# Kernel optimization log

Measured on AMD Instinct MI355X. Metric: run time of the kernel, lower is better.

Reference implementation:

```python
import jax, jax.numpy as jnp
import numpy as np


def setup_inputs() -> dict:
    key = jax.random.key(0)
    k1, k2, k3, k4 = jax.random.split(key, 4)
    B, T, E, D = 4, 4096, 2048, 128
    x = jax.random.normal(k1, (B, T, E), dtype=jnp.float32)
    # nn.Linear(E, D, bias=False): y = x @ W where W is [E, D]
    scale = 1.0 / np.sqrt(E)
    Wq = jax.random.normal(k2, (E, D), dtype=jnp.float32) * scale
    Wk = jax.random.normal(k3, (E, D), dtype=jnp.float32) * scale
    Wv = jax.random.normal(k4, (E, D), dtype=jnp.float32) * scale
    return {"x": x, "Wq": Wq, "Wk": Wk, "Wv": Wv}


def reference(x, Wq, Wk, Wv):
    # Single attention head, prefill path (kv_cache=None, T_q == T_k).
    D = Wq.shape[1]
    Q = jnp.einsum('bte,ed->btd', x, Wq)
    K = jnp.einsum('bte,ed->btd', x, Wk)
    V = jnp.einsum('bte,ed->btd', x, Wv)
    scores = jnp.einsum('bqd,bkd->bqk', Q, K) / jnp.sqrt(jnp.float32(D))
    T = x.shape[1]
    causal = jnp.tril(jnp.ones((T, T), dtype=bool))  # [T_q, T_k]
    scores = jnp.where(causal[None, :, :], scores, -jnp.inf)
    attn = jax.nn.softmax(scores, axis=-1)
    out = jnp.einsum('bqk,bkd->bqd', attn, V)
    return out
```

## Files before the change

### kernel.cpp

```cpp
#include <hip/hip_runtime.h>
#include <hip/hip_bf16.h>

typedef short bf16x8 __attribute__((ext_vector_type(8)));
typedef float f32x4  __attribute__((ext_vector_type(4)));

#define T_SEQ 4096
#define NB    4
#define E_DIM 2048
#define D_DIM 128
#define M_TOT (NB * T_SEQ)
#define NCHUNK 4
#define CHUNK_KT 16
#define SM_SHIFT 12.0f

__device__ __forceinline__ ushort f2bf(float f) {
  union { float f; unsigned u; } c; c.f = f;
  unsigned u = c.u;
  unsigned r = (u + 0x7FFFu + ((u >> 16) & 1u)) >> 16;
  return (ushort)r;
}
__device__ __forceinline__ float bf2f(ushort u) {
  union { unsigned u; float f; } c; c.u = ((unsigned)u) << 16;
  return c.f;
}
__device__ __forceinline__ bf16x8 cvt8(const float4& lo, const float4& hi) {
  union { __hip_bfloat162 h; ushort u[2]; } t;
  union { ushort u[8]; bf16x8 v; } r;
  t.h = __float22bfloat162_rn(make_float2(lo.x, lo.y)); r.u[0] = t.u[0]; r.u[1] = t.u[1];
  t.h = __float22bfloat162_rn(make_float2(lo.z, lo.w)); r.u[2] = t.u[0]; r.u[3] = t.u[1];
  t.h = __float22bfloat162_rn(make_float2(hi.x, hi.y)); r.u[4] = t.u[0]; r.u[5] = t.u[1];
  t.h = __float22bfloat162_rn(make_float2(hi.z, hi.w)); r.u[6] = t.u[0]; r.u[7] = t.u[1];
  return r.v;
}

__device__ __forceinline__ void gl2lds16(const void* g, void* l) {
  __builtin_amdgcn_global_load_lds(
      (const __attribute__((address_space(1))) unsigned int*)g,
      (__attribute__((address_space(3))) unsigned int*)l, 16, 0, 0);
}

__global__ __launch_bounds__(256) void build_wt(const float* __restrict__ Wq,
                                                const float* __restrict__ Wk,
                                                const float* __restrict__ Wv,
                                                ushort* __restrict__ Wt) {
  __shared__ ushort tile[64][72];
  const int tid = threadIdx.x;
  const int k0 = blockIdx.x * 64, n0 = blockIdx.y * 64, o = blockIdx.z;
  const float* W = (o == 0) ? Wq : ((o == 1) ? Wk : Wv);
  for (int i = 0; i < 4; i++) {
    int c = tid + i * 256;
    int r = c >> 4, c4 = (c & 15) * 4;
    float4 v = *(const float4*)(W + (size_t)(k0 + r) * D_DIM + n0 + c4);
    ushort4 b4;
    b4.x = f2bf(v.x); b4.y = f2bf(v.y); b4.z = f2bf(v.z); b4.w = f2bf(v.w);
    *(ushort4*)(&tile[r][c4]) = b4;
  }
  __syncthreads();
  for (int i = 0; i < 2; i++) {
    int c = tid + i * 256;
    int nn = c >> 3, k8 = (c & 7) * 8;
    ushort tmp[8];
    for (int j = 0; j < 8; j++) tmp[j] = tile[k8 + j][nn];
    *(uint4*)(Wt + (size_t)((o << 7) + n0 + nn) * E_DIM + k0 + k8) = *(const uint4*)tmp;
  }
}

__global__ __launch_bounds__(256, 4) void qkv_gemm(const float* __restrict__ x,
                                                   const ushort* __restrict__ Wt,
                                                   ushort* __restrict__ Q,
                                                   ushort* __restrict__ K,
                                                   ushort* __restrict__ Vt) {
  __shared__ ushort As[2][64 * 64];
  __shared__ ushort Bs[2][96 * 64];

  const int tid  = threadIdx.x;
  const int wave = tid >> 6, lane = tid & 63;
  const int quad = lane >> 4, l16 = lane & 15;
  const int wm = wave >> 1, wn = wave & 1;
  const int m0 = blockIdx.x * 64;
  const int n0 = blockIdx.y * 96;

  f32x4 acc[2][3] = {};

  const int s_ = wave * 64 + lane;
  const int n_ = s_ >> 3, p_ = s_ & 7;

  const int ar_ = tid >> 2, aq4_ = tid & 3;
  const float* xrow = x + (size_t)(m0 + ar_) * E_DIM + aq4_ * 16;

#define DMA_B(k0_, buf_)                                                        \
  _Pragma("unroll")                                                             \
  for (int i_ = 0; i_ < 3; i_++) {                                              \
    int slotbase = i_ * 256 + wave * 64;                                        \
    int n = (i_ * 32) + n_;                           \
    int cg = p_ ^ (n & 7);                                                      \
    gl2lds16(Wt + (size_t)(n0 + n) * E_DIM + (k0_) + cg * 8,                    \
             (char*)(buf_) + (size_t)slotbase * 16);                            \
  }

#define GLOAD_A(k0_)                                                            \
  {                                                                             \
    const float* ap_ = xrow + (k0_);                                            \
    areg0 = *(const float4*)(ap_);                                              \
    areg1 = *(const float4*)(ap_ + 4);                                          \
    areg2 = *(const float4*)(ap_ + 8);                                          \
    areg3 = *(const float4*)(ap_ + 12);                                         \
  }

#define CVT_WRITE_A(bufidx)                                                     \
  {                                                                             \
    ushort* as_ = As[bufidx];                                                   \
    bf16x8 w0_ = cvt8(areg0, areg1);                                            \
    bf16x8 w1_ = cvt8(areg2, areg3);                                            \
    *(bf16x8*)(as_ + ar_ * 64 + (((aq4_ * 2)     ^ (ar_ & 7)) * 8)) = w0_;      \
    *(bf16x8*)(as_ + ar_ * 64 + (((aq4_ * 2 + 1) ^ (ar_ & 7)) * 8)) = w1_;      \
  }

#define COMPUTE(bufidx)                                                         \
  {                                                                             \
    const ushort* as_ = As[bufidx];                                             \
    const ushort* bs_ = Bs[bufidx];                                             \
    _Pragma("unroll")                                                           \
    for (int kk = 0; kk < 2; kk++) {                                            \
      const int slot = ((kk * 4 + quad) ^ (l16 & 7)) * 8;                       \
      bf16x8 af0 = *(const bf16x8*)(as_ + (wm * 32 + l16) * 64 + slot);         \
      bf16x8 af1 = *(const bf16x8*)(as_ + (wm * 32 + 16 + l16) * 64 + slot);    \
      _Pragma("unroll")                                                         \
      for (int ni = 0; ni < 3; ni++) {                                          \
        int n = wn * 48 + ni * 16 + l16;                                        \
        bf16x8 bf = *(const bf16x8*)(bs_ + n * 64 + slot);                      \
        acc[0][ni] = __builtin_amdgcn_mfma_f32_16x16x32_bf16(af0, bf, acc[0][ni], 0, 0, 0); \
        acc[1][ni] = __builtin_amdgcn_mfma_f32_16x16x32_bf16(af1, bf, acc[1][ni], 0, 0, 0); \
      }                                                                         \
    }                                                                           \
  }

  float4 areg0, areg1, areg2, areg3;

  GLOAD_A(0);
  DMA_B(0, Bs[0]);
  CVT_WRITE_A(0);
  __syncthreads();

  for (int it = 0; it < 32; it += 2) {
    GLOAD_A((it + 1) * 64);
    DMA_B((it + 1) * 64, Bs[1]);
    COMPUTE(0);
    CVT_WRITE_A(1);
    __syncthreads();
    if (it < 30) {
      GLOAD_A((it + 2) * 64);
      DMA_B((it + 2) * 64, Bs[0]);
      COMPUTE(1);
      CVT_WRITE_A(0);
      __syncthreads();
    } else {
      COMPUTE(1);
    }
  }

  const int b  = m0 >> 12;
  const int t0 = m0 & 4095;
  const int dbase2 = (n0 == 192) ? 0 : 32;
  ushort* vtile = (ushort*)As;

  __syncthreads();

  for (int mi = 0; mi < 2; mi++)
    for (int ni = 0; ni < 3; ni++) {
      int colall = n0 + wn * 48 + ni * 16 + l16;
      int o = colall >> 7, d = colall & 127;
      if (o < 2) {
        ushort* dst = o ? K : Q;
        for (int r = 0; r < 4; r++) {
          int row = m0 + wm * 32 + mi * 16 + quad * 4 + r;
          dst[(size_t)row * D_DIM + d] = f2bf(acc[mi][ni][r]);
        }
      } else {
        int dloc = d - dbase2;
        for (int r = 0; r < 4; r++) {
          int mloc = wm * 32 + mi * 16 + quad * 4 + r;
          vtile[dloc * 72 + mloc] = f2bf(acc[mi][ni][r]);
        }
      }
    }

  if (n0 >= 192) {
    __syncthreads();
    const int nrows = (n0 == 192) ? 32 : 96;
    if (tid < nrows * 2) {
      int dloc = tid >> 1, half = tid & 1;
      const ushort* src = vtile + dloc * 72 + half * 32;
      ushort* dstp = Vt + (size_t)(b * D_DIM + dbase2 + dloc) * T_SEQ + t0 + half * 32;
#pragma unroll
      for (int j = 0; j < 4; j++)
        ((uint4*)dstp)[j] = ((const uint4*)src)[j];
    }
  }
#undef DMA_B
#undef GLOAD_A
#undef CVT_WRITE_A
#undef COMPUTE
}

__global__ __launch_bounds__(256, 2) void attn_partial(const ushort* __restrict__ Q,
                                                       const ushort* __restrict__ K,
                                                       const ushort* __restrict__ Vt,
                                                       ushort* __restrict__ Po,
                                                       float* __restrict__ Ll) {
  const int qt = blockIdx.x, cq = blockIdx.y, b = blockIdx.z;
  const int kt0 = cq * CHUNK_KT;
  if (kt0 > qt) return;

  __shared__ ushort Kt[2][64 * 128];
  __shared__ ushort Vts[2][128 * 64];
  __shared__ ushort Pls[4][16][72];

  const int tid = threadIdx.x;
  const int wave = tid >> 6, lane = tid & 63;
  const int quad = lane >> 4, l16 = lane & 15;

  const ushort* Kb  = K  + (size_t)b * T_SEQ * D_DIM;
  const ushort* Vtb = Vt + (size_t)b * D_DIM * T_SEQ;

  const int skn_ = tid >> 4, skp_ = tid & 15;
  const int svd_ = tid >> 3, svp_ = tid & 7;

#define DMA_K(kt_, buf_)                                                        \
  _Pragma("unroll")                                                             \
  for (int i_ = 0; i_ < 4; i_++) {                                              \
    int slotbase = i_ * 256 + wave * 64;                                        \
    int n = i_ * 16 + skn_;                                                     \
    int cg = skp_ ^ (n & 7);                                                    \
    gl2lds16(Kb + (size_t)((kt_) * 64 + n) * D_DIM + cg * 8,                    \
             (char*)(Kt[buf_]) + (size_t)slotbase * 16);                        \
  }

#define DMA_V(kt_, buf_)                                                        \
  _Pragma("unroll")                                                             \
  for (int i_ = 0; i_ < 4; i_++) {                                              \
    int slotbase = i_ * 256 + wave * 64;                                        \
    int d = i_ * 32 + svd_;                                                     \
    int cg = svp_ ^ (d & 7);                                                    \
    gl2lds16(Vtb + (size_t)d * T_SEQ + (kt_) * 64 + cg * 8,                     \
             (char*)(Vts[buf_]) + (size_t)slotbase * 16);                       \
  }

  const int qrow = qt * 64 + wave * 16 + l16;
  bf16x8 qf[4];
#pragma unroll
  for (int kk = 0; kk < 4; kk++)
    qf[kk] = *(const bf16x8*)(Q + (size_t)(b * T_SEQ + qrow) * D_DIM + kk * 32 + quad * 8);

  bf16x8 ones;
#pragma unroll
  for (int j = 0; j < 8; j++) ones[j] = (short)0x3F80;

  f32x4 o_acc[8] = {};
  f32x4 lacc = {};
  const float scale2 = 0.08838834764831845f * 1.4426950408889634f;

  const int kt1 = min(qt, kt0 + CHUNK_KT - 1);

  DMA_K(kt0, 0);
  DMA_V(kt0, 0);
  __syncthreads();

  for (int kt = kt0; kt <= kt1; kt++) {
    const int cur = (kt - kt0) & 1;
    if (kt < kt1) { DMA_K(kt + 1, cur ^ 1); DMA_V(kt + 1, cur ^ 1); }
    const ushort* kts = Kt[cur];
    const ushort* vts = Vts[cur];

    f32x4 s[4] = {};
#pragma unroll
    for (int kk = 0; kk < 4; kk++) {
#pragma unroll
      for (int ni = 0; ni < 4; ni++) {
        int row = ni * 16 + l16;
        int pg = (kk * 4 + quad) ^ (row & 7);
        bf16x8 bf = *(const bf16x8*)(kts + row * 128 + pg * 8);
        s[ni] = __builtin_amdgcn_mfma_f32_16x16x32_bf16(qf[kk], bf, s[ni], 0, 0, 0);
      }
    }
    if (kt == qt) {
#pragma unroll
      for (int ni = 0; ni < 4; ni++) {
        int kidx = kt * 64 + ni * 16 + l16;
#pragma unroll
        for (int r = 0; r < 4; r++) {
          int qidx = qt * 64 + wave * 16 + quad * 4 + r;
          float v = (kidx > qidx) ? -1e30f : (s[ni][r] * scale2 - SM_SHIFT);
          s[ni][r] = exp2f(v);
        }
      }
    } else {
#pragma unroll
      for (int ni = 0; ni < 4; ni++)
#pragma unroll
        for (int r = 0; r < 4; r++)
          s[ni][r] = exp2f(s[ni][r] * scale2 - SM_SHIFT);
    }
#pragma unroll
    for (int ni = 0; ni < 4; ni++)
#pragma unroll
      for (int r = 0; r < 4; r++)
        Pls[wave][quad * 4 + r][ni * 16 + l16] = f2bf(s[ni][r]);
#pragma unroll
    for (int kk2 = 0; kk2 < 2; kk2++) {
      const int kc = kk2 * 32 + quad * 8;
      bf16x8 pf = *(const bf16x8*)(&Pls[wave][l16][kc]);
#pragma unroll
      for (int ni = 0; ni < 8; ni++) {
        int row = ni * 16 + l16;
        int pg = (kk2 * 4 + quad) ^ (row & 7);
        bf16x8 vf = *(const bf16x8*)(vts + row * 64 + pg * 8);
        o_acc[ni] = __builtin_amdgcn_mfma_f32_16x16x32_bf16(pf, vf, o_acc[ni], 0, 0, 0);
      }
      lacc = __builtin_amdgcn_mfma_f32_16x16x32_bf16(pf, ones, lacc, 0, 0, 0);
    }

    __syncthreads();
  }

  const int slot = (b * 64 + qt) * NCHUNK + cq;
#pragma unroll
  for (int ni = 0; ni < 8; ni++)
#pragma unroll
    for (int r = 0; r < 4; r++) {
      int ql = wave * 16 + quad * 4 + r;
      Po[(size_t)slot * 8192 + ql * D_DIM + ni * 16 + l16] = f2bf(o_acc[ni][r]);
    }
  if (l16 == 0) {
#pragma unroll
    for (int r = 0; r < 4; r++) {
      int ql = wave * 16 + quad * 4 + r;
      Ll[slot * 64 + ql] = lacc[r];
    }
  }
#undef DMA_K
#undef DMA_V
}

__global__ __launch_bounds__(256) void attn_reduce(const ushort* __restrict__ Po,
                                                   const float* __restrict__ Ll,
                                                   float* __restrict__ out) {
  const int qt = blockIdx.x, b = blockIdx.y;
  const int nc = qt / CHUNK_KT + 1;
  const int tid = threadIdx.x;
  const int row = tid >> 2;
  const int c0  = (tid & 3) * 32;
  const int base_slot = (b * 64 + qt) * NCHUNK;

  float L = 0.f;
  for (int c = 0; c < nc; c++) L += Ll[(base_slot + c) * 64 + row];
  const float inv = 1.0f / L;

  const size_t orow = (size_t)(b * T_SEQ + qt * 64 + row) * D_DIM;
  for (int cc = 0; cc < 32; cc += 8) {
    float a[8] = {0,0,0,0,0,0,0,0};
    for (int c = 0; c < nc; c++) {
      const ushort* p = Po + (size_t)(base_slot + c) * 8192 + row * D_DIM + c0 + cc;
      ushort u[8];
      *(uint4*)u = *(const uint4*)p;
      for (int j = 0; j < 8; j++) a[j] += bf2f(u[j]);
    }
    float4 o0, o1;
    o0.x = a[0] * inv; o0.y = a[1] * inv; o0.z = a[2] * inv; o0.w = a[3] * inv;
    o1.x = a[4] * inv; o1.y = a[5] * inv; o1.z = a[6] * inv; o1.w = a[7] * inv;
    *(float4*)(out + orow + c0 + cc)     = o0;
    *(float4*)(out + orow + c0 + cc + 4) = o1;
  }
}

extern "C" void kernel_launch(void* const* d_in, const int* in_sizes, int n_in,
                              void* d_out, int out_size, void* d_ws, size_t ws_size,
                              hipStream_t stream) {
  const float* x  = (const float*)d_in[0];
  const float* Wq = (const float*)d_in[1];
  const float* Wk = (const float*)d_in[2];
  const float* Wv = (const float*)d_in[3];
  float* out = (float*)d_out;

  ushort* Q  = (ushort*)d_ws;
  ushort* Kb = Q  + (size_t)M_TOT * D_DIM;
  ushort* Vb = Kb + (size_t)M_TOT * D_DIM;
  ushort* Vt = Vb + (size_t)M_TOT * D_DIM;
  ushort* Wt = Vt + (size_t)M_TOT * D_DIM;
  ushort* Po = Wt + (size_t)384 * E_DIM;
  float*  Ll = (float*)(Po + (size_t)NB * 64 * NCHUNK * 8192);

  hipLaunchKernelGGL(build_wt,     dim3(32, 2, 3),       dim3(256), 0, stream, Wq, Wk, Wv, Wt);
  hipLaunchKernelGGL(qkv_gemm,     dim3(256, 4),         dim3(256), 0, stream, x, Wt, Q, Kb, Vt);
  hipLaunchKernelGGL(attn_partial, dim3(64, NCHUNK, 4),  dim3(256), 0, stream, Q, Kb, Vt, Po, Ll);
  hipLaunchKernelGGL(attn_reduce,  dim3(64, 4),          dim3(256), 0, stream, Po, Ll, out);
}
```

Before: 306.1 us.

## Pre-convert x to bf16 and single-buffer attention K/V for higher occupancy

Adds a separate pass converting x from fp32 to bf16 in workspace. A new GEMM variant then streams A tiles via async global-to-LDS copies, avoiding repeated fp32 loads and conversion in each N-tile block. The attention partial kernel drops double-buffered K/V in favour of single buffers with occupancy 4 and a swizzled P staging layout. This adds a conversion pass and extra workspace, and loses load/compute overlap in attention. The new GEMM path is used only when the workspace is large enough.

```diff
diff --git a/kernel.cpp b/kernel.cpp
--- a/kernel.cpp
+++ b/kernel.cpp
@@ -65,11 +65,23 @@
   }
 }
 
-__global__ __launch_bounds__(256, 4) void qkv_gemm(const float* __restrict__ x,
-                                                   const ushort* __restrict__ Wt,
-                                                   ushort* __restrict__ Q,
-                                                   ushort* __restrict__ K,
-                                                   ushort* __restrict__ Vt) {
+__global__ __launch_bounds__(256) void x_cvt(const float* __restrict__ x,
+                                             ushort* __restrict__ xbf) {
+  const size_t n8 = (size_t)M_TOT * E_DIM / 8;
+  const size_t stride = (size_t)gridDim.x * 256;
+  for (size_t i = (size_t)blockIdx.x * 256 + threadIdx.x; i < n8; i += stride) {
+    const float* p = x + i * 8;
+    float4 lo = *(const float4*)p;
+    float4 hi = *(const float4*)(p + 4);
+    *(bf16x8*)(xbf + i * 8) = cvt8(lo, hi);
+  }
+}
+
+__global__ __launch_bounds__(256, 4) void qkv_gemm_bf(const ushort* __restrict__ xbf,
+                                                      const ushort* __restrict__ Wt,
+                                                      ushort* __restrict__ Q,
+                                                      ushort* __restrict__ K,
+                                                      ushort* __restrict__ Vt) {
   __shared__ ushort As[2][64 * 64];
   __shared__ ushort Bs[2][96 * 64];
 
@@ -84,36 +96,27 @@
 
   const int s_ = wave * 64 + lane;
   const int n_ = s_ >> 3, p_ = s_ & 7;
-
-  const int ar_ = tid >> 2, aq4_ = tid & 3;
-  const float* xrow = x + (size_t)(m0 + ar_) * E_DIM + aq4_ * 16;
+  const int arow_ = wave * 8 + (lane >> 3);
+  const int ap_ = lane & 7;
 
 #define DMA_B(k0_, buf_)                                                        \
   _Pragma("unroll")                                                             \
   for (int i_ = 0; i_ < 3; i_++) {                                              \
     int slotbase = i_ * 256 + wave * 64;                                        \
-    int n = (i_ * 32) + n_;                           \
+    int n = (i_ * 32) + n_;                                                     \
     int cg = p_ ^ (n & 7);                                                      \
     gl2lds16(Wt + (size_t)(n0 + n) * E_DIM + (k0_) + cg * 8,                    \
              (char*)(buf_) + (size_t)slotbase * 16);                            \
   }
 
-#define GLOAD_A(k0_)                                                            \
-  {                                                                             \
-    const float* ap_ = xrow + (k0_);                                            \
-    areg0 = *(const float4*)(ap_);                                              \
-    areg1 = *(const float4*)(ap_ + 4);                                          \
-    areg2 = *(const float4*)(ap_ + 8);                                          \
-    areg3 = *(const float4*)(ap_ + 12);                                         \
-  }
-
-#define CVT_WRITE_A(bufidx)                                                     \
-  {                                                                             \
-    ushort* as_ = As[bufidx];                                                   \
-    bf16x8 w0_ = cvt8(areg0, areg1);                                            \
-    bf16x8 w1_ = cvt8(areg2, areg3);                                            \
-    *(bf16x8*)(as_ + ar_ * 64 + (((aq4_ * 2)     ^ (ar_ & 7)) * 8)) = w0_;      \
-    *(bf16x8*)(as_ + ar_ * 64 + (((aq4_ * 2 + 1) ^ (ar_ & 7)) * 8)) = w1_;      \
+#define DMA_A(k0_, buf_)                                                        \
+  _Pragma("unroll")                                                             \
+  for (int i_ = 0; i_ < 2; i_++) {                                              \
+    int slotbase = i_ * 256 + wave * 64;                                        \
+    int row = i_ * 32 + arow_;                                                  \
+    int cg = ap_ ^ (row & 7);                                                   \
+    gl2lds16(xbf + (size_t)(m0 + row) * E_DIM + (k0_) + cg * 8,                 \
+             (char*)(buf_) + (size_t)slotbase * 16);                            \
   }
 
 #define COMPUTE(bufidx)                                                         \
@@ -135,28 +138,17 @@
     }                                                                           \
   }
 
-  float4 areg0, areg1, areg2, areg3;
-
-  GLOAD_A(0);
+  DMA_A(0, As[0]);
   DMA_B(0, Bs[0]);
-  CVT_WRITE_A(0);
   __syncthreads();
 
-  for (int it = 0; it < 32; it += 2) {
-    GLOAD_A((it + 1) * 64);
-    DMA_B((it + 1) * 64, Bs[1]);
-    COMPUTE(0);
-    CVT_WRITE_A(1);
+  for (int it = 0; it < 32; it++) {
+    if (it < 31) {
+      DMA_A((it + 1) * 64, As[(it + 1) & 1]);
+      DMA_B((it + 1) * 64, Bs[(it + 1) & 1]);
+    }
+    COMPUTE(it & 1);
     __syncthreads();
-    if (it < 30) {
-      GLOAD_A((it + 2) * 64);
-      DMA_B((it + 2) * 64, Bs[0]);
-      COMPUTE(1);
-      CVT_WRITE_A(0);
-      __syncthreads();
-    } else {
-      COMPUTE(1);
-    }
   }
 
   const int b  = m0 >> 12;
@@ -198,12 +190,148 @@
     }
   }
 #undef DMA_B
+#undef DMA_A
+#undef COMPUTE
+}
+
+__global__ __launch_bounds__(256, 4) void qkv_gemm(const float* __restrict__ x,
+                                                   const ushort* __restrict__ Wt,
+                                                   ushort* __restrict__ Q,
+                                                   ushort* __restrict__ K,
+                                                   ushort* __restrict__ Vt) {
+  __shared__ ushort As[2][64 * 64];
+  __shared__ ushort Bs[2][96 * 64];
+
+  const int tid  = threadIdx.x;
+  const int wave = tid >> 6, lane = tid & 63;
+  const int quad = lane >> 4, l16 = lane & 15;
+  const int wm = wave >> 1, wn = wave & 1;
+  const int m0 = blockIdx.x * 64;
+  const int n0 = blockIdx.y * 96;
+
+  f32x4 acc[2][3] = {};
+
+  const int s_ = wave * 64 + lane;
+  const int n_ = s_ >> 3, p_ = s_ & 7;
+  const int ar_ = tid >> 2, aq4_ = tid & 3;
+  const float* xrow = x + (size_t)(m0 + ar_) * E_DIM + aq4_ * 16;
+
+#define DMA_B(k0_, buf_)                                                        \
+  _Pragma("unroll")                                                             \
+  for (int i_ = 0; i_ < 3; i_++) {                                              \
+    int slotbase = i_ * 256 + wave * 64;                                        \
+    int n = (i_ * 32) + n_;                                                     \
+    int cg = p_ ^ (n & 7);                                                      \
+    gl2lds16(Wt + (size_t)(n0 + n) * E_DIM + (k0_) + cg * 8,                    \
+             (char*)(buf_) + (size_t)slotbase * 16);                            \
+  }
+
+#define GLOAD_A(k0_)                                                            \
+  {                                                                             \
+    const float* ap_ = xrow + (k0_);                                            \
+    areg0 = *(const float4*)(ap_);                                              \
+    areg1 = *(const float4*)(ap_ + 4);                                          \
+    areg2 = *(const float4*)(ap_ + 8);                                          \
+    areg3 = *(const float4*)(ap_ + 12);                                         \
+  }
+
+#define CVT_WRITE_A(bufidx)                                                     \
+  {                                                                             \
+    ushort* as_ = As[bufidx];                                                   \
+    bf16x8 w0_ = cvt8(areg0, areg1);                                            \
+    bf16x8 w1_ = cvt8(areg2, areg3);                                            \
+    *(bf16x8*)(as_ + ar_ * 64 + (((aq4_ * 2)     ^ (ar_ & 7)) * 8)) = w0_;      \
+    *(bf16x8*)(as_ + ar_ * 64 + (((aq4_ * 2 + 1) ^ (ar_ & 7)) * 8)) = w1_;      \
+  }
+
+#define COMPUTE(bufidx)                                                         \
+  {                                                                             \
+    const ushort* as_ = As[bufidx];                                             \
+    const ushort* bs_ = Bs[bufidx];                                             \
+    _Pragma("unroll")                                                           \
+    for (int kk = 0; kk < 2; kk++) {                                            \
+      const int slot = ((kk * 4 + quad) ^ (l16 & 7)) * 8;                       \
+      bf16x8 af0 = *(const bf16x8*)(as_ + (wm * 32 + l16) * 64 + slot);         \
+      bf16x8 af1 = *(const bf16x8*)(as_ + (wm * 32 + 16 + l16) * 64 + slot);    \
+      _Pragma("unroll")                                                         \
+      for (int ni = 0; ni < 3; ni++) {                                          \
+        int n = wn * 48 + ni * 16 + l16;                                        \
+        bf16x8 bf = *(const bf16x8*)(bs_ + n * 64 + slot);                      \
+        acc[0][ni] = __builtin_amdgcn_mfma_f32_16x16x32_bf16(af0, bf, acc[0][ni], 0, 0, 0); \
+        acc[1][ni] = __builtin_amdgcn_mfma_f32_16x16x32_bf16(af1, bf, acc[1][ni], 0, 0, 0); \
+      }                                                                         \
+    }                                                                           \
+  }
+
+  float4 areg0, areg1, areg2, areg3;
+
+  GLOAD_A(0);
+  DMA_B(0, Bs[0]);
+  CVT_WRITE_A(0);
+  __syncthreads();
+
+  for (int it = 0; it < 32; it += 2) {
+    GLOAD_A((it + 1) * 64);
+    DMA_B((it + 1) * 64, Bs[1]);
+    COMPUTE(0);
+    CVT_WRITE_A(1);
+    __syncthreads();
+    if (it < 30) {
+      GLOAD_A((it + 2) * 64);
+      DMA_B((it + 2) * 64, Bs[0]);
+      COMPUTE(1);
+      CVT_WRITE_A(0);
+      __syncthreads();
+    } else {
+      COMPUTE(1);
+    }
+  }
+
+  const int b  = m0 >> 12;
+  const int t0 = m0 & 4095;
+  const int dbase2 = (n0 == 192) ? 0 : 32;
+  ushort* vtile = (ushort*)As;
+
+  __syncthreads();
+
+  for (int mi = 0; mi < 2; mi++)
+    for (int ni = 0; ni < 3; ni++) {
+      int colall = n0 + wn * 48 + ni * 16 + l16;
+      int o = colall >> 7, d = colall & 127;
+      if (o < 2) {
+        ushort* dst = o ? K : Q;
+        for (int r = 0; r < 4; r++) {
+          int row = m0 + wm * 32 + mi * 16 + quad * 4 + r;
+          dst[(size_t)row * D_DIM + d] = f2bf(acc[mi][ni][r]);
+        }
+      } else {
+        int dloc = d - dbase2;
+        for (int r = 0; r < 4; r++) {
+          int mloc = wm * 32 + mi * 16 + quad * 4 + r;
+          vtile[dloc * 72 + mloc] = f2bf(acc[mi][ni][r]);
+        }
+      }
+    }
+
+  if (n0 >= 192) {
+    __syncthreads();
+    const int nrows = (n0 == 192) ? 32 : 96;
+    if (tid < nrows * 2) {
+      int dloc = tid >> 1, half = tid & 1;
+      const ushort* src = vtile + dloc * 72 + half * 32;
+      ushort* dstp = Vt + (size_t)(b * D_DIM + dbase2 + dloc) * T_SEQ + t0 + half * 32;
+#pragma unroll
+      for (int j = 0; j < 4; j++)
+        ((uint4*)dstp)[j] = ((const uint4*)src)[j];
+    }
+  }
+#undef DMA_B
 #undef GLOAD_A
 #undef CVT_WRITE_A
 #undef COMPUTE
 }
 
-__global__ __launch_bounds__(256, 2) void attn_partial(const ushort* __restrict__ Q,
+__global__ __launch_bounds__(256, 4) void attn_partial(const ushort* __restrict__ Q,
                                                        const ushort* __restrict__ K,
                                                        const ushort* __restrict__ Vt,
                                                        ushort* __restrict__ Po,
@@ -212,9 +340,9 @@
   const int kt0 = cq * CHUNK_KT;
   if (kt0 > qt) return;
 
-  __shared__ ushort Kt[2][64 * 128];
-  __shared__ ushort Vts[2][128 * 64];
-  __shared__ ushort Pls[4][16][72];
+  __shared__ ushort Kt[64 * 128];
+  __shared__ ushort Vts[128 * 64];
+  __shared__ ushort Pls[4][16 * 64];
 
   const int tid = threadIdx.x;
   const int wave = tid >> 6, lane = tid & 63;
@@ -226,24 +354,24 @@
   const int skn_ = tid >> 4, skp_ = tid & 15;
   const int svd_ = tid >> 3, svp_ = tid & 7;
 
-#define DMA_K(kt_, buf_)                                                        \
+#define DMA_K(kt_)                                                              \
   _Pragma("unroll")                                                             \
   for (int i_ = 0; i_ < 4; i_++) {                                              \
     int slotbase = i_ * 256 + wave * 64;                                        \
     int n = i_ * 16 + skn_;                                                     \
     int cg = skp_ ^ (n & 7);                                                    \
     gl2lds16(Kb + (size_t)((kt_) * 64 + n) * D_DIM + cg * 8,                    \
-             (char*)(Kt[buf_]) + (size_t)slotbase * 16);                        \
-  }
-
-#define DMA_V(kt_, buf_)                                                        \
+             (char*)Kt + (size_t)slotbase * 16);                                \
+  }
+
+#define DMA_V(kt_)                                                              \
   _Pragma("unroll")                                                             \
   for (int i_ = 0; i_ < 4; i_++) {                                              \
     int slotbase = i_ * 256 + wave * 64;                                        \
     int d = i_ * 32 + svd_;                                                     \
     int cg = svp_ ^ (d & 7);                                                    \
     gl2lds16(Vtb + (size_t)d * T_SEQ + (kt_) * 64 + cg * 8,                     \
-             (char*)(Vts[buf_]) + (size_t)slotbase * 16);                       \
+             (char*)Vts + (size_t)slotbase * 16);                               \
   }
 
   const int qrow = qt * 64 + wave * 16 + l16;
@@ -262,15 +390,11 @@
 
   const int kt1 = min(qt, kt0 + CHUNK_KT - 1);
 
-  DMA_K(kt0, 0);
-  DMA_V(kt0, 0);
-  __syncthreads();
-
   for (int kt = kt0; kt <= kt1; kt++) {
-    const int cur = (kt - kt0) & 1;
-    if (kt < kt1) { DMA_K(kt + 1, cur ^ 1); DMA_V(kt + 1, cur ^ 1); }
-    const ushort* kts = Kt[cur];
-    const ushort* vts = Vts[cur];
+    __syncthreads();
+    DMA_K(kt);
+    DMA_V(kt);
+    __syncthreads();
 
     f32x4 s[4] = {};
 #pragma unroll
@@ -279,7 +403,7 @@
       for (int ni = 0; ni < 4; ni++) {
         int row = ni * 16 + l16;
         int pg = (kk * 4 + quad) ^ (row & 7);
-        bf16x8 bf = *(const bf16x8*)(kts + row * 128 + pg * 8);
+        bf16x8 bf = *(const bf16x8*)(Kt + row * 128 + pg * 8);
         s[ni] = __builtin_amdgcn_mfma_f32_16x16x32_bf16(qf[kk], bf, s[ni], 0, 0, 0);
       }
     }
@@ -304,23 +428,23 @@
 #pragma unroll
     for (int ni = 0; ni < 4; ni++)
 #pragma unroll
-      for (int r = 0; r < 4; r++)
-        Pls[wave][quad * 4 + r][ni * 16 + l16] = f2bf(s[ni][r]);
+      for (int r = 0; r < 4; r++) {
+        int row = quad * 4 + r;
+        int col = ni * 16 + l16;
+        Pls[wave][row * 64 + (((col >> 3) ^ (row & 7)) * 8) + (col & 7)] = f2bf(s[ni][r]);
+      }
 #pragma unroll
     for (int kk2 = 0; kk2 < 2; kk2++) {
-      const int kc = kk2 * 32 + quad * 8;
-      bf16x8 pf = *(const bf16x8*)(&Pls[wave][l16][kc]);
+      bf16x8 pf = *(const bf16x8*)(&Pls[wave][l16 * 64 + (((kk2 * 4 + quad) ^ (l16 & 7)) * 8)]);
 #pragma unroll
       for (int ni = 0; ni < 8; ni++) {
         int row = ni * 16 + l16;
         int pg = (kk2 * 4 + quad) ^ (row & 7);
-        bf16x8 vf = *(const bf16x8*)(vts + row * 64 + pg * 8);
+        bf16x8 vf = *(const bf16x8*)(Vts + row * 64 + pg * 8);
         o_acc[ni] = __builtin_amdgcn_mfma_f32_16x16x32_bf16(pf, vf, o_acc[ni], 0, 0, 0);
       }
       lacc = __builtin_amdgcn_mfma_f32_16x16x32_bf16(pf, ones, lacc, 0, 0, 0);
     }
-
-    __syncthreads();
   }
 
   const int slot = (b * 64 + qt) * NCHUNK + cq;
@@ -389,9 +513,17 @@
   ushort* Wt = Vt + (size_t)M_TOT * D_DIM;
   ushort* Po = Wt + (size_t)384 * E_DIM;
   float*  Ll = (float*)(Po + (size_t)NB * 64 * NCHUNK * 8192);
-
-  hipLaunchKernelGGL(build_wt,     dim3(32, 2, 3),       dim3(256), 0, stream, Wq, Wk, Wv, Wt);
-  hipLaunchKernelGGL(qkv_gemm,     dim3(256, 4),         dim3(256), 0, stream, x, Wt, Q, Kb, Vt);
-  hipLaunchKernelGGL(attn_partial, dim3(64, NCHUNK, 4),  dim3(256), 0, stream, Q, Kb, Vt, Po, Ll);
-  hipLaunchKernelGGL(attn_reduce,  dim3(64, 4),          dim3(256), 0, stream, Po, Ll, out);
-}
+  ushort* xbf = (ushort*)(Ll + (size_t)NB * 64 * NCHUNK * 64);
+
+  const size_t needed = (size_t)((char*)(xbf + (size_t)M_TOT * E_DIM) - (char*)d_ws);
+
+  hipLaunchKernelGGL(build_wt, dim3(32, 2, 3), dim3(256), 0, stream, Wq, Wk, Wv, Wt);
+  if (ws_size >= needed) {
+    hipLaunchKernelGGL(x_cvt,       dim3(2048),   dim3(256), 0, stream, x, xbf);
+    hipLaunchKernelGGL(qkv_gemm_bf, dim3(256, 4), dim3(256), 0, stream, xbf, Wt, Q, Kb, Vt);
+  } else {
+    hipLaunchKernelGGL(qkv_gemm,    dim3(256, 4), dim3(256), 0, stream, x, Wt, Q, Kb, Vt);
+  }
+  hipLaunchKernelGGL(attn_partial, dim3(64, NCHUNK, 4), dim3(256), 0, stream, Q, Kb, Vt, Po, Ll);
+  hipLaunchKernelGGL(attn_reduce,  dim3(64, 4),         dim3(256), 0, stream, Po, Ll, out);
+}
```

New measurement: 302.7 us. Within noise of the previous version (-1.1%).
